# Optimization experiments

Hardware: AMD Instinct MI355X
Metric: run time of the kernel (lower is better)

## Reference

```python
import jax, jax.numpy as jnp
import numpy as np
from math import sqrt

DIM = 2048
NUM_HEADS = 16
HEAD_DIM = DIM // NUM_HEADS
BSZ, SEQ = 2, 2048


def setup_inputs() -> dict:
    key = jax.random.key(0)
    kx, kq, kk, kv, ko = jax.random.split(key, 5)
    x = jax.random.normal(kx, (BSZ, SEQ, DIM), dtype=jnp.float32)
    # causal additive mask, broadcastable to [B, H, S, S]
    neg = jnp.finfo(jnp.float32).min
    mask = jnp.where(jnp.tril(jnp.ones((SEQ, SEQ), dtype=bool)), 0.0, neg)[None, None]
    s = 1.0 / sqrt(DIM)
    Wq = jax.random.normal(kq, (DIM, DIM), dtype=jnp.float32) * s
    Wk = jax.random.normal(kk, (DIM, DIM), dtype=jnp.float32) * s
    Wv = jax.random.normal(kv, (DIM, DIM), dtype=jnp.float32) * s
    Wo = jax.random.normal(ko, (DIM, DIM), dtype=jnp.float32) * s
    return {"x": x, "mask": mask, "Wq": Wq, "Wk": Wk, "Wv": Wv, "Wo": Wo}


def reference(x, mask, Wq, Wk, Wv, Wo):
    b, s, _ = x.shape
    # nn.Linear: y = x @ W.T
    def proj(W):
        return (x @ W.T).reshape(b, s, NUM_HEADS, HEAD_DIM).transpose(0, 2, 1, 3)  # [b,h,s,d]
    q, k, v = proj(Wq), proj(Wk), proj(Wv)
    scores = jnp.einsum('bhqd,bhkd->bhqk', q, k) / sqrt(HEAD_DIM)
    scores = scores + mask
    attn = jax.nn.softmax(scores.astype(jnp.float32), axis=-1).astype(q.dtype)
    out = jnp.einsum('bhqk,bhkd->bhqd', attn, v)
    out = out.transpose(0, 2, 1, 3).reshape(b, s, -1)
    return out @ Wo.T
```

## Files before the change

kernel.cpp:

```cpp
#include <hip/hip_runtime.h>
#include <hip/hip_bf16.h>
#include <stdint.h>

#define DIM 2048
#define NHEADS 16
#define HDIM 128
#define BATCH 2
#define SEQLEN 2048

using bf16x8 = __attribute__((ext_vector_type(8))) __bf16;
using f32x4  = __attribute__((ext_vector_type(4))) float;
typedef unsigned short u16;
typedef unsigned int u32;

__device__ __forceinline__ void cp16(const void* g, void* lds) {
  __builtin_amdgcn_global_load_lds((const __attribute__((address_space(1))) u32*)g,
                                   (__attribute__((address_space(3))) u32*)lds, 16, 0, 0);
}

__device__ __forceinline__ u16 f2b(float f) {
  u32 u = __float_as_uint(f);
  return (u16)((u + 0x7fffu + ((u >> 16) & 1u)) >> 16);
}

__global__ __launch_bounds__(256) void cvt_kernel(
    const float* __restrict__ x,
    const float* __restrict__ Wq, const float* __restrict__ Wk,
    const float* __restrict__ Wv, const float* __restrict__ Wo,
    u16* __restrict__ xb, u16* __restrict__ wqb, u16* __restrict__ wkb,
    u16* __restrict__ wvb, u16* __restrict__ wob)
{
  const size_t Wsz = (size_t)DIM * DIM;
  const float* src; u16* dst;
  switch (blockIdx.y) {
    case 0:  src = x;        dst = xb;        break;
    case 1:  src = x + Wsz;  dst = xb + Wsz;  break;
    case 2:  src = Wq;       dst = wqb;       break;
    case 3:  src = Wk;       dst = wkb;       break;
    case 4:  src = Wv;       dst = wvb;       break;
    default: src = Wo;       dst = wob;       break;
  }
  size_t i = ((size_t)blockIdx.x * 256 + threadIdx.x) * 8;
  float4 a = *(const float4*)(src + i);
  float4 b = *(const float4*)(src + i + 4);
  union { bf16x8 v; u16 s[8]; } u;
  u.s[0] = f2b(a.x); u.s[1] = f2b(a.y); u.s[2] = f2b(a.z); u.s[3] = f2b(a.w);
  u.s[4] = f2b(b.x); u.s[5] = f2b(b.y); u.s[6] = f2b(b.z); u.s[7] = f2b(b.w);
  *(bf16x8*)(dst + i) = u.v;
}

template<bool HEADED, bool COUTF32>
__device__ __forceinline__ void gemm_body(const u16* __restrict__ A, const u16* __restrict__ B,
                                          void* Cp, u16* As, u16* Bs)
{
  const int tid = threadIdx.x;
  const int w = tid >> 6, l = tid & 63;
  const int wm = w >> 1, wn = w & 1;
  const int quad = l >> 4, ln = l & 15;
  const int bm = blockIdx.y, bn = blockIdx.x;

  f32x4 acc[4][4];
#pragma unroll
  for (int i = 0; i < 4; ++i)
#pragma unroll
    for (int j = 0; j < 4; ++j) acc[i][j] = (f32x4){0.f, 0.f, 0.f, 0.f};

  const u16* Ag = A + (size_t)(bm * 128 + (tid >> 2)) * DIM + (tid & 3) * 8;
  const u16* Bg = B + (size_t)(bn * 128 + (tid >> 2)) * DIM + (tid & 3) * 8;
  u16* AsW = As + w * 512;
  u16* BsW = Bs + w * 512;

  for (int k0 = 0; k0 < DIM; k0 += 32) {
    cp16(Ag + k0, AsW);
    cp16(Ag + k0 + 64 * DIM, AsW + 2048);
    cp16(Bg + k0, BsW);
    cp16(Bg + k0 + 64 * DIM, BsW + 2048);
    __syncthreads();

    bf16x8 af[4], bfr[4];
#pragma unroll
    for (int mi = 0; mi < 4; ++mi)
      af[mi] = *(const bf16x8*)(As + (wm * 64 + mi * 16 + ln) * 32 + quad * 8);
#pragma unroll
    for (int ni = 0; ni < 4; ++ni)
      bfr[ni] = *(const bf16x8*)(Bs + (wn * 64 + ni * 16 + ln) * 32 + quad * 8);
#pragma unroll
    for (int mi = 0; mi < 4; ++mi)
#pragma unroll
      for (int ni = 0; ni < 4; ++ni)
        acc[mi][ni] = __builtin_amdgcn_mfma_f32_16x16x32_bf16(af[mi], bfr[ni], acc[mi][ni], 0, 0, 0);
    __syncthreads();
  }

#pragma unroll
  for (int mi = 0; mi < 4; ++mi)
#pragma unroll
    for (int ni = 0; ni < 4; ++ni)
#pragma unroll
      for (int r = 0; r < 4; ++r) {
        int i = bm * 128 + wm * 64 + mi * 16 + quad * 4 + r;
        int j = bn * 128 + wn * 64 + ni * 16 + ln;
        size_t off;
        if (HEADED) {
          int b = i >> 11, s = i & 2047, h = j >> 7, d = j & 127;
          off = ((size_t)((b * NHEADS + h) * SEQLEN + s)) * HDIM + d;
        } else {
          off = (size_t)i * DIM + j;
        }
        if constexpr (COUTF32) ((float*)Cp)[off] = acc[mi][ni][r];
        else                   ((u16*)Cp)[off]   = f2b(acc[mi][ni][r]);
      }
}

__global__ __launch_bounds__(256) void qkv_kernel(const u16* __restrict__ xb,
    const u16* __restrict__ Wq, const u16* __restrict__ Wk, const u16* __restrict__ Wv,
    u16* __restrict__ Q, u16* __restrict__ Kk, u16* __restrict__ V)
{
  __shared__ __align__(16) u16 As[128 * 32];
  __shared__ __align__(16) u16 Bs[128 * 32];
  const u16* B; u16* C;
  if (blockIdx.z == 0)      { B = Wq; C = Q; }
  else if (blockIdx.z == 1) { B = Wk; C = Kk; }
  else                      { B = Wv; C = V; }
  gemm_body<true, false>(xb, B, C, As, Bs);
}

__global__ __launch_bounds__(256) void out_kernel(const u16* __restrict__ ctx,
    const u16* __restrict__ Wo, float* __restrict__ out)
{
  __shared__ __align__(16) u16 As[128 * 32];
  __shared__ __align__(16) u16 Bs[128 * 32];
  gemm_body<false, true>(ctx, Wo, out, As, Bs);
}

__global__ __launch_bounds__(256, 2) void attn_kernel(const u16* __restrict__ Q,
    const u16* __restrict__ K, const u16* __restrict__ V, u16* __restrict__ ctx)
{
  __shared__ __align__(16) u16 Ks[64 * 128];
  __shared__ __align__(16) u16 Vt[128 * 72];
  __shared__ __align__(16) u16 Ps[4][32 * 64];

  const int tid = threadIdx.x;
  const int w = tid >> 6, l = tid & 63;
  const int quad = l >> 4, ln = l & 15;

  const int j = blockIdx.x;
  const int b = j >> 8;
  const int kk = j & 255;
  const int h = kk >> 4;
  const int q0 = kk & 15;
  const int qt = b ? (15 - q0) : q0;

  const size_t head_off = (size_t)(b * NHEADS + h) * SEQLEN * HDIM;
  const u16* Qg = Q + head_off + (size_t)qt * 128 * HDIM;

  const int swsrc = (tid * 8) ^ (((tid >> 4) & 7) << 3);
  const int swr = (ln & 7) << 3;

  bf16x8 aq[2][4];
#pragma unroll
  for (int chunk = 0; chunk < 2; ++chunk) {
    u16* base = Ks + w * 512;
    const u16* g = Qg + chunk * 8192 + swsrc;
    cp16(g, base); cp16(g + 2048, base + 2048);
    cp16(g + 4096, base + 4096); cp16(g + 6144, base + 6144);
    __syncthreads();
    if ((w >> 1) == chunk) {
      int rl = (w & 1) * 32;
#pragma unroll
      for (int mi = 0; mi < 2; ++mi)
#pragma unroll
        for (int kb = 0; kb < 4; ++kb)
          aq[mi][kb] = *(const bf16x8*)(Ks + (((rl + mi * 16 + ln) * 128 + kb * 32 + quad * 8) ^ swr));
    }
    __syncthreads();
  }

  float m_run[2][4], l_run[2][4];
  f32x4 o[2][8];
#pragma unroll
  for (int mi = 0; mi < 2; ++mi) {
#pragma unroll
    for (int r = 0; r < 4; ++r) { m_run[mi][r] = -1e30f; l_run[mi][r] = 0.f; }
#pragma unroll
    for (int cb = 0; cb < 8; ++cb) o[mi][cb] = (f32x4){0.f, 0.f, 0.f, 0.f};
  }

  const float c2 = 0.08838834764831845f * 1.4426950408889634f;

  const int NT = 2 * qt + 2;
  for (int ct = 0; ct < NT; ++ct) {
    const u16* Kg = K + head_off + (size_t)ct * 64 * HDIM;
    const u16* Vg = V + head_off + (size_t)ct * 64 * HDIM;
    {
      u16* base = Ks + w * 512;
      const u16* g = Kg + swsrc;
      cp16(g, base); cp16(g + 2048, base + 2048);
      cp16(g + 4096, base + 4096); cp16(g + 6144, base + 6144);
    }
#pragma unroll
    for (int c = 0; c < 2; ++c) {
      int u = c * 256 + tid;
      int rp = u & 31, db = u >> 5;
      int t0 = rp * 2;
      uint4 ra = *(const uint4*)(Vg + t0 * 128 + db * 8);
      uint4 rb = *(const uint4*)(Vg + (t0 + 1) * 128 + db * 8);
      const u16* pa = (const u16*)&ra;
      const u16* pb = (const u16*)&rb;
#pragma unroll
      for (int e = 0; e < 8; ++e) {
        int d = db * 8 + e;
        *(u32*)&Vt[d * 72 + t0] = (u32)pa[e] | ((u32)pb[e] << 16);
      }
    }
    __syncthreads();

    const bool active = !(ct == 2 * qt + 1 && w < 2);

    if (active) {
      f32x4 sc[2][4];
#pragma unroll
      for (int mi = 0; mi < 2; ++mi)
#pragma unroll
        for (int nb = 0; nb < 4; ++nb) sc[mi][nb] = (f32x4){0.f, 0.f, 0.f, 0.f};
#pragma unroll
      for (int kb = 0; kb < 4; ++kb) {
        bf16x8 bk[4];
#pragma unroll
        for (int nb = 0; nb < 4; ++nb)
          bk[nb] = *(const bf16x8*)(Ks + (((nb * 16 + ln) * 128 + kb * 32 + quad * 8) ^ swr));
#pragma unroll
        for (int mi = 0; mi < 2; ++mi)
#pragma unroll
          for (int nb = 0; nb < 4; ++nb)
            sc[mi][nb] = __builtin_amdgcn_mfma_f32_16x16x32_bf16(aq[mi][kb], bk[nb], sc[mi][nb], 0, 0, 0);
      }

      if (ct >= 2 * qt) {
        int d = (2 * qt - ct) * 64;
#pragma unroll
        for (int mi = 0; mi < 2; ++mi)
#pragma unroll
          for (int nb = 0; nb < 4; ++nb) {
            int col = nb * 16 + ln;
#pragma unroll
            for (int r = 0; r < 4; ++r) {
              int row = w * 32 + mi * 16 + quad * 4 + r;
              if (col > row + d) sc[mi][nb][r] = -1e30f;
            }
          }
      }

#pragma unroll
      for (int mi = 0; mi < 2; ++mi)
#pragma unroll
        for (int r = 0; r < 4; ++r) {
          float mx = fmaxf(fmaxf(sc[mi][0][r], sc[mi][1][r]), fmaxf(sc[mi][2][r], sc[mi][3][r]));
#pragma unroll
          for (int s = 1; s < 16; s <<= 1) mx = fmaxf(mx, __shfl_xor(mx, s, 64));
          float mnew = fmaxf(m_run[mi][r], mx);
          float sum = 0.f;
          float p[4];
#pragma unroll
          for (int nb = 0; nb < 4; ++nb) {
            p[nb] = exp2f((sc[mi][nb][r] - mnew) * c2);
            sum += p[nb];
          }
#pragma unroll
          for (int s = 1; s < 16; s <<= 1) sum += __shfl_xor(sum, s, 64);
          float alpha = exp2f((m_run[mi][r] - mnew) * c2);
          l_run[mi][r] = l_run[mi][r] * alpha + sum;
          m_run[mi][r] = mnew;
#pragma unroll
          for (int cb = 0; cb < 8; ++cb) o[mi][cb][r] *= alpha;
          int row = mi * 16 + quad * 4 + r;
#pragma unroll
          for (int nb = 0; nb < 4; ++nb)
            Ps[w][(row * 64 + nb * 16 + ln) ^ ((row & 7) << 3)] = f2b(p[nb]);
        }
    }

    __syncthreads();

    if (active) {
#pragma unroll
      for (int tb = 0; tb < 2; ++tb) {
        bf16x8 ap[2];
#pragma unroll
        for (int mi = 0; mi < 2; ++mi)
          ap[mi] = *(const bf16x8*)(&Ps[w][0] + (((mi * 16 + ln) * 64 + tb * 32 + quad * 8) ^ swr));
#pragma unroll
        for (int cb = 0; cb < 8; ++cb) {
          bf16x8 bv = *(const bf16x8*)(Vt + (cb * 16 + ln) * 72 + tb * 32 + quad * 8);
#pragma unroll
          for (int mi = 0; mi < 2; ++mi)
            o[mi][cb] = __builtin_amdgcn_mfma_f32_16x16x32_bf16(ap[mi], bv, o[mi][cb], 0, 0, 0);
        }
      }
    }
    __syncthreads();
  }

#pragma unroll
  for (int mi = 0; mi < 2; ++mi)
#pragma unroll
    for (int cb = 0; cb < 8; ++cb)
#pragma unroll
      for (int r = 0; r < 4; ++r) {
        float v = o[mi][cb][r] / l_run[mi][r];
        int srow = qt * 128 + w * 32 + mi * 16 + quad * 4 + r;
        size_t off = ((size_t)(b * SEQLEN + srow)) * DIM + h * HDIM + cb * 16 + ln;
        ctx[off] = f2b(v);
      }
}

extern "C" void kernel_launch(void* const* d_in, const int* in_sizes, int n_in,
                              void* d_out, int out_size, void* d_ws, size_t ws_size,
                              hipStream_t stream) {
  const float* x  = (const float*)d_in[0];
  const float* Wq = (const float*)d_in[2];
  const float* Wk = (const float*)d_in[3];
  const float* Wv = (const float*)d_in[4];
  const float* Wo = (const float*)d_in[5];
  float* out = (float*)d_out;

  const size_t HSZ = (size_t)BATCH * NHEADS * SEQLEN * HDIM;
  const size_t WSZ = (size_t)DIM * DIM;
  u16* Qw  = (u16*)d_out;
  u16* xb  = Qw + HSZ;
  u16* wqb = (u16*)d_ws;
  u16* wkb = wqb + WSZ;
  u16* wvb = wkb + WSZ;
  u16* wob = wvb + WSZ;
  u16* Kw  = wob + WSZ;
  u16* Vw  = Kw + HSZ;
  u16* Cw  = Vw + HSZ;

  cvt_kernel<<<dim3(WSZ / (256 * 8), 6), 256, 0, stream>>>(
      x, Wq, Wk, Wv, Wo, xb, wqb, wkb, wvb, wob);
  qkv_kernel<<<dim3(DIM / 128, (BATCH * SEQLEN) / 128, 3), 256, 0, stream>>>(
      xb, wqb, wkb, wvb, Qw, Kw, Vw);
  attn_kernel<<<dim3(BATCH * NHEADS * (SEQLEN / 128)), 256, 0, stream>>>(Qw, Kw, Vw, Cw);
  out_kernel<<<dim3(DIM / 128, (BATCH * SEQLEN) / 128, 1), 256, 0, stream>>>(Cw, wob, out);
}
```

Baseline: 446.9 us.

## Store V transposed from QKV GEMM and double-buffer K/V tiles in attention

The QKV GEMM now writes V in a per-head transposed [d][seq] layout, so the attention kernel can load V tiles straight into LDS with async global-to-LDS copies instead of transposing them through registers. K and V tiles are double-buffered so the next tile's loads overlap the current tile's compute, with explicit vmcnt waits and raw barriers. The intra-tile barrier between the softmax P write and the PV MFMA is replaced by a per-wave lgkmcnt wait, since each wave only reads its own P buffer. This doubles K/V LDS use, which may limit occupancy, and the hand-placed waitcnt counts are fragile.

```diff
diff --git a/kernel.cpp b/kernel.cpp
--- a/kernel.cpp
+++ b/kernel.cpp
@@ -49,7 +49,7 @@
   *(bf16x8*)(dst + i) = u.v;
 }
 
-template<bool HEADED, bool COUTF32>
+template<int OM>
 __device__ __forceinline__ void gemm_body(const u16* __restrict__ A, const u16* __restrict__ B,
                                           void* Cp, u16* As, u16* Bs)
 {
@@ -92,24 +92,38 @@
     __syncthreads();
   }
 
-#pragma unroll
-  for (int mi = 0; mi < 4; ++mi)
-#pragma unroll
-    for (int ni = 0; ni < 4; ++ni)
-#pragma unroll
-      for (int r = 0; r < 4; ++r) {
-        int i = bm * 128 + wm * 64 + mi * 16 + quad * 4 + r;
-        int j = bn * 128 + wn * 64 + ni * 16 + ln;
-        size_t off;
-        if (HEADED) {
-          int b = i >> 11, s = i & 2047, h = j >> 7, d = j & 127;
-          off = ((size_t)((b * NHEADS + h) * SEQLEN + s)) * HDIM + d;
-        } else {
-          off = (size_t)i * DIM + j;
+  if constexpr (OM == 2) {
+#pragma unroll
+    for (int mi = 0; mi < 4; ++mi)
+#pragma unroll
+      for (int ni = 0; ni < 4; ++ni) {
+        int i0 = bm * 128 + wm * 64 + mi * 16 + quad * 4;
+        int jj = bn * 128 + wn * 64 + ni * 16 + ln;
+        int b = i0 >> 11, s0 = i0 & 2047, hh = jj >> 7, d = jj & 127;
+        ushort4 v4;
+        v4.x = f2b(acc[mi][ni][0]); v4.y = f2b(acc[mi][ni][1]);
+        v4.z = f2b(acc[mi][ni][2]); v4.w = f2b(acc[mi][ni][3]);
+        size_t off = ((size_t)((b * NHEADS + hh) * HDIM + d)) * SEQLEN + s0;
+        *(ushort4*)((u16*)Cp + off) = v4;
+      }
+  } else {
+#pragma unroll
+    for (int mi = 0; mi < 4; ++mi)
+#pragma unroll
+      for (int ni = 0; ni < 4; ++ni)
+#pragma unroll
+        for (int r = 0; r < 4; ++r) {
+          int i = bm * 128 + wm * 64 + mi * 16 + quad * 4 + r;
+          int jj = bn * 128 + wn * 64 + ni * 16 + ln;
+          if constexpr (OM == 1) {
+            int b = i >> 11, s = i & 2047, hh = jj >> 7, d = jj & 127;
+            size_t off = ((size_t)((b * NHEADS + hh) * SEQLEN + s)) * HDIM + d;
+            ((u16*)Cp)[off] = f2b(acc[mi][ni][r]);
+          } else {
+            ((float*)Cp)[(size_t)i * DIM + jj] = acc[mi][ni][r];
+          }
         }
-        if constexpr (COUTF32) ((float*)Cp)[off] = acc[mi][ni][r];
-        else                   ((u16*)Cp)[off]   = f2b(acc[mi][ni][r]);
-      }
+  }
 }
 
 __global__ __launch_bounds__(256) void qkv_kernel(const u16* __restrict__ xb,
@@ -118,11 +132,9 @@
 {
   __shared__ __align__(16) u16 As[128 * 32];
   __shared__ __align__(16) u16 Bs[128 * 32];
-  const u16* B; u16* C;
-  if (blockIdx.z == 0)      { B = Wq; C = Q; }
-  else if (blockIdx.z == 1) { B = Wk; C = Kk; }
-  else                      { B = Wv; C = V; }
-  gemm_body<true, false>(xb, B, C, As, Bs);
+  if (blockIdx.z == 0)      gemm_body<1>(xb, Wq, Q, As, Bs);
+  else if (blockIdx.z == 1) gemm_body<1>(xb, Wk, Kk, As, Bs);
+  else                      gemm_body<2>(xb, Wv, V, As, Bs);
 }
 
 __global__ __launch_bounds__(256) void out_kernel(const u16* __restrict__ ctx,
@@ -130,14 +142,14 @@
 {
   __shared__ __align__(16) u16 As[128 * 32];
   __shared__ __align__(16) u16 Bs[128 * 32];
-  gemm_body<false, true>(ctx, Wo, out, As, Bs);
+  gemm_body<0>(ctx, Wo, out, As, Bs);
 }
 
 __global__ __launch_bounds__(256, 2) void attn_kernel(const u16* __restrict__ Q,
-    const u16* __restrict__ K, const u16* __restrict__ V, u16* __restrict__ ctx)
-{
-  __shared__ __align__(16) u16 Ks[64 * 128];
-  __shared__ __align__(16) u16 Vt[128 * 72];
+    const u16* __restrict__ K, const u16* __restrict__ VT, u16* __restrict__ ctx)
+{
+  __shared__ __align__(16) u16 Ks[2][64 * 128];
+  __shared__ __align__(16) u16 Vt[2][128 * 64];
   __shared__ __align__(16) u16 Ps[4][32 * 64];
 
   const int tid = threadIdx.x;
@@ -153,14 +165,19 @@
 
   const size_t head_off = (size_t)(b * NHEADS + h) * SEQLEN * HDIM;
   const u16* Qg = Q + head_off + (size_t)qt * 128 * HDIM;
+  const u16* Kh = K + head_off;
+  const u16* Vh = VT + head_off;
 
   const int swsrc = (tid * 8) ^ (((tid >> 4) & 7) << 3);
   const int swr = (ln & 7) << 3;
 
+  const int vrow = w * 8 + (l >> 3);
+  const int vcol = (((l & 7) ^ (l >> 3)) << 3);
+
   bf16x8 aq[2][4];
 #pragma unroll
   for (int chunk = 0; chunk < 2; ++chunk) {
-    u16* base = Ks + w * 512;
+    u16* base = Ks[0] + w * 512;
     const u16* g = Qg + chunk * 8192 + swsrc;
     cp16(g, base); cp16(g + 2048, base + 2048);
     cp16(g + 4096, base + 4096); cp16(g + 6144, base + 6144);
@@ -171,7 +188,7 @@
       for (int mi = 0; mi < 2; ++mi)
 #pragma unroll
         for (int kb = 0; kb < 4; ++kb)
-          aq[mi][kb] = *(const bf16x8*)(Ks + (((rl + mi * 16 + ln) * 128 + kb * 32 + quad * 8) ^ swr));
+          aq[mi][kb] = *(const bf16x8*)(Ks[0] + (((rl + mi * 16 + ln) * 128 + kb * 32 + quad * 8) ^ swr));
     }
     __syncthreads();
   }
@@ -187,35 +204,40 @@
   }
 
   const float c2 = 0.08838834764831845f * 1.4426950408889634f;
-
   const int NT = 2 * qt + 2;
+
+  {
+    u16* kb_ = Ks[0] + w * 512;
+    const u16* kg = Kh + swsrc;
+    cp16(kg, kb_); cp16(kg + 2048, kb_ + 2048);
+    cp16(kg + 4096, kb_ + 4096); cp16(kg + 6144, kb_ + 6144);
+    u16* vb_ = Vt[0] + w * 512;
+    const u16* vg = Vh + (size_t)vrow * SEQLEN + vcol;
+    cp16(vg, vb_); cp16(vg + 32 * SEQLEN, vb_ + 2048);
+    cp16(vg + 64 * SEQLEN, vb_ + 4096); cp16(vg + 96 * SEQLEN, vb_ + 6144);
+  }
+
+  int cur = 0;
   for (int ct = 0; ct < NT; ++ct) {
-    const u16* Kg = K + head_off + (size_t)ct * 64 * HDIM;
-    const u16* Vg = V + head_off + (size_t)ct * 64 * HDIM;
-    {
-      u16* base = Ks + w * 512;
-      const u16* g = Kg + swsrc;
-      cp16(g, base); cp16(g + 2048, base + 2048);
-      cp16(g + 4096, base + 4096); cp16(g + 6144, base + 6144);
+    if (ct + 1 < NT) {
+      u16* kb_ = Ks[cur ^ 1] + w * 512;
+      const u16* kg = Kh + (size_t)(ct + 1) * 64 * HDIM + swsrc;
+      cp16(kg, kb_); cp16(kg + 2048, kb_ + 2048);
+      cp16(kg + 4096, kb_ + 4096); cp16(kg + 6144, kb_ + 6144);
+      u16* vb_ = Vt[cur ^ 1] + w * 512;
+      const u16* vg = Vh + (size_t)vrow * SEQLEN + (ct + 1) * 64 + vcol;
+      cp16(vg, vb_); cp16(vg + 32 * SEQLEN, vb_ + 2048);
+      cp16(vg + 64 * SEQLEN, vb_ + 4096); cp16(vg + 96 * SEQLEN, vb_ + 6144);
+      asm volatile("s_waitcnt vmcnt(8)" ::: "memory");
+    } else {
+      asm volatile("s_waitcnt vmcnt(0)" ::: "memory");
     }
-#pragma unroll
-    for (int c = 0; c < 2; ++c) {
-      int u = c * 256 + tid;
-      int rp = u & 31, db = u >> 5;
-      int t0 = rp * 2;
-      uint4 ra = *(const uint4*)(Vg + t0 * 128 + db * 8);
-      uint4 rb = *(const uint4*)(Vg + (t0 + 1) * 128 + db * 8);
-      const u16* pa = (const u16*)&ra;
-      const u16* pb = (const u16*)&rb;
-#pragma unroll
-      for (int e = 0; e < 8; ++e) {
-        int d = db * 8 + e;
-        *(u32*)&Vt[d * 72 + t0] = (u32)pa[e] | ((u32)pb[e] << 16);
-      }
-    }
-    __syncthreads();
-
-    const bool active = !(ct == 2 * qt + 1 && w < 2);
+    __builtin_amdgcn_s_barrier();
+    __builtin_amdgcn_sched_barrier(0);
+
+    const u16* KsC = Ks[cur];
+    const u16* VtC = Vt[cur];
+    const bool active = !(ct == NT - 1 && w < 2);
 
     if (active) {
       f32x4 sc[2][4];
@@ -228,7 +250,7 @@
         bf16x8 bk[4];
 #pragma unroll
         for (int nb = 0; nb < 4; ++nb)
-          bk[nb] = *(const bf16x8*)(Ks + (((nb * 16 + ln) * 128 + kb * 32 + quad * 8) ^ swr));
+          bk[nb] = *(const bf16x8*)(KsC + (((nb * 16 + ln) * 128 + kb * 32 + quad * 8) ^ swr));
 #pragma unroll
         for (int mi = 0; mi < 2; ++mi)
 #pragma unroll
@@ -237,7 +259,7 @@
       }
 
       if (ct >= 2 * qt) {
-        int d = (2 * qt - ct) * 64;
+        int dd = (2 * qt - ct) * 64;
 #pragma unroll
         for (int mi = 0; mi < 2; ++mi)
 #pragma unroll
@@ -246,7 +268,7 @@
 #pragma unroll
             for (int r = 0; r < 4; ++r) {
               int row = w * 32 + mi * 16 + quad * 4 + r;
-              if (col > row + d) sc[mi][nb][r] = -1e30f;
+              if (col > row + dd) sc[mi][nb][r] = -1e30f;
             }
           }
       }
@@ -278,11 +300,11 @@
           for (int nb = 0; nb < 4; ++nb)
             Ps[w][(row * 64 + nb * 16 + ln) ^ ((row & 7) << 3)] = f2b(p[nb]);
         }
-    }
-
-    __syncthreads();
-
-    if (active) {
+
+      __builtin_amdgcn_sched_barrier(0);
+      asm volatile("s_waitcnt lgkmcnt(0)" ::: "memory");
+      __builtin_amdgcn_sched_barrier(0);
+
 #pragma unroll
       for (int tb = 0; tb < 2; ++tb) {
         bf16x8 ap[2];
@@ -291,14 +313,18 @@
           ap[mi] = *(const bf16x8*)(&Ps[w][0] + (((mi * 16 + ln) * 64 + tb * 32 + quad * 8) ^ swr));
 #pragma unroll
         for (int cb = 0; cb < 8; ++cb) {
-          bf16x8 bv = *(const bf16x8*)(Vt + (cb * 16 + ln) * 72 + tb * 32 + quad * 8);
+          bf16x8 bv = *(const bf16x8*)(VtC + ((cb * 16 + ln) * 64 + ((tb * 32 + quad * 8) ^ swr)));
 #pragma unroll
           for (int mi = 0; mi < 2; ++mi)
             o[mi][cb] = __builtin_amdgcn_mfma_f32_16x16x32_bf16(ap[mi], bv, o[mi][cb], 0, 0, 0);
         }
       }
     }
-    __syncthreads();
+
+    __builtin_amdgcn_sched_barrier(0);
+    asm volatile("s_waitcnt lgkmcnt(0)" ::: "memory");
+    __builtin_amdgcn_s_barrier();
+    cur ^= 1;
   }
 
 #pragma unroll
```

After: 448.2 us. No clear change (+0.3%).
